# Optimization experiments

Measured on AMD Instinct MI355X. Metric: run time of the kernel, lower is better.

The kernel has to match this reference:

```python
import jax, jax.numpy as jnp
import numpy as np

N_NODES = 100000
N_EDGES = 3200000
IN_CH = 32
HID = 16


def setup_inputs() -> dict:
    key = jax.random.key(0)
    ks = jax.random.split(key, 8)
    x = jax.random.normal(ks[0], (N_NODES, IN_CH), dtype=jnp.float32)
    edge_index = jax.random.randint(ks[1], (2, N_EDGES), 0, N_NODES, dtype=jnp.int64)
    s1 = 1.0 / np.sqrt(IN_CH)
    s2 = 1.0 / np.sqrt(HID)
    Wl1 = jax.random.normal(ks[2], (HID, IN_CH), dtype=jnp.float32) * s1
    Wr1 = jax.random.normal(ks[3], (HID, IN_CH), dtype=jnp.float32) * s1
    b1 = jnp.zeros((HID,), dtype=jnp.float32)
    Wl2 = jax.random.normal(ks[4], (1, HID), dtype=jnp.float32) * s2
    Wr2 = jax.random.normal(ks[5], (1, HID), dtype=jnp.float32) * s2
    b2 = jnp.zeros((1,), dtype=jnp.float32)
    return {"x": x, "edge_index": edge_index, "Wl1": Wl1, "Wr1": Wr1,
            "b1": b1, "Wl2": Wl2, "Wr2": Wr2, "b2": b2}


def _sage_conv(h, src, dst, deg_inv, Wl, Wr, b):
    # mean aggregation of source features at destination nodes
    msg_sum = jax.ops.segment_sum(h[src], dst, num_segments=N_NODES)  # [N, F]
    agg = msg_sum * deg_inv[:, None]
    # lin_l(agg) + lin_r(h): lin_l carries the bias (PyG SAGEConv convention)
    return agg @ Wl.T + b + h @ Wr.T


def reference(x, edge_index, Wl1, Wr1, b1, Wl2, Wr2, b2):
    src = edge_index[0]
    dst = edge_index[1]
    deg = jax.ops.segment_sum(jnp.ones((N_EDGES,), dtype=x.dtype), dst,
                              num_segments=N_NODES)
    deg_inv = 1.0 / jnp.maximum(deg, 1.0)  # mean; nodes w/o in-edges get 0 agg

    h = _sage_conv(x, src, dst, deg_inv, Wl1, Wr1, b1)
    h = jax.nn.relu(h)
    # F.dropout in eval mode -> identity
    out = _sage_conv(h, src, dst, deg_inv, Wl2, Wr2, b2)
    return out.squeeze(-1)  # [N]
```

## Files before the change

### kernel.cpp

```cpp
#include <hip/hip_runtime.h>

#define N_NODES 100000
#define N_EDGES 3200000
#define NB 1024
#define BKN 98
#define RSZ 3968
#define TILE 6250
#define NTILES 512
#define MAXIT 13
#define MAXB 8


__device__ __forceinline__ float bf2f_lo(unsigned int w) {
  return __uint_as_float(w << 16);
}
__device__ __forceinline__ float bf2f_hi(unsigned int w) {
  return __uint_as_float(w & 0xFFFF0000u);
}
__device__ __forceinline__ unsigned short f2bf(float f) {
  unsigned int b = __float_as_uint(f);
  return (unsigned short)((b + 0x7FFFu + ((b >> 16) & 1u)) >> 16);
}

__global__ __launch_bounds__(256) void k_proj1(
    const float* __restrict__ x, const float* __restrict__ Wl1,
    const float* __restrict__ Wr1, const float* __restrict__ b1,
    unsigned short* __restrict__ p1h, float* __restrict__ q1b,
    int* __restrict__ gcur) {
  __shared__ float sWl[512];
  __shared__ float sWr[512];
  __shared__ float sb[16];
  const int t = threadIdx.x;
  if (t < 64) {
    const int gi = blockIdx.x * 64 + t;
    if (gi < NB * 16) gcur[gi] = 0;
  }
  for (int i = t; i < 512; i += 256) {
    sWl[i] = Wl1[i];
    sWr[i] = Wr1[i];
  }
  if (t < 16) sb[t] = b1[t];
  __syncthreads();

  const int n = blockIdx.x * 256 + t;
  if (n >= N_NODES) return;

  float xr[32];
  const float4* xp = (const float4*)(x + (size_t)n * 32);
#pragma unroll
  for (int j = 0; j < 8; ++j) {
    float4 v = xp[j];
    xr[4 * j + 0] = v.x;
    xr[4 * j + 1] = v.y;
    xr[4 * j + 2] = v.z;
    xr[4 * j + 3] = v.w;
  }
  float pv[16], qv[16];
#pragma unroll
  for (int hh = 0; hh < 16; ++hh) {
    float a = 0.f, b = 0.f;
#pragma unroll
    for (int i = 0; i < 32; ++i) {
      a = fmaf(xr[i], sWl[hh * 32 + i], a);
      b = fmaf(xr[i], sWr[hh * 32 + i], b);
    }
    pv[hh] = a;
    qv[hh] = b + sb[hh];
  }
  unsigned int w[8];
#pragma unroll
  for (int j = 0; j < 8; ++j)
    w[j] = (unsigned int)f2bf(pv[2 * j]) |
           ((unsigned int)f2bf(pv[2 * j + 1]) << 16);
  uint4* pp = (uint4*)(p1h + (size_t)n * 16);
  pp[0] = make_uint4(w[0], w[1], w[2], w[3]);
  pp[1] = make_uint4(w[4], w[5], w[6], w[7]);
  float4* qp = (float4*)(q1b + (size_t)n * 16);
#pragma unroll
  for (int j = 0; j < 4; ++j)
    qp[j] = make_float4(qv[4 * j], qv[4 * j + 1], qv[4 * j + 2], qv[4 * j + 3]);
}

__global__ __launch_bounds__(512) void k_bscatter(const int* __restrict__ ei,
                                                  int* __restrict__ gcur,
                                                  int* __restrict__ recs) {
  __shared__ int hist[1024];
  __shared__ int delta[NB];
  __shared__ int seg[512];
  __shared__ int stage[TILE];
  __shared__ unsigned short bid[TILE + 6];
  const int t = threadIdx.x;
  for (int i = t; i < 1024; i += 512) hist[i] = 0;
  __syncthreads();

  const int tb = blockIdx.x * TILE;
  int rec[MAXIT], aux[MAXIT];
#pragma unroll
  for (int i = 0; i < MAXIT; ++i) {
    const int pos = t + i * 512;
    if (pos < TILE) {
      const int e = tb + pos;
      const int s = ei[e];
      const int d = ei[N_EDGES + e];
      const int k = (int)((unsigned)d / (unsigned)BKN);
      const int rank = atomicAdd(&hist[k], 1);
      rec[i] = ((d - k * BKN) << 17) | s;
      aux[i] = (k << 16) | rank;
    } else {
      aux[i] = -1;
    }
  }
  __syncthreads();

  const int s0 = hist[2 * t], s1 = hist[2 * t + 1];
  const int my = s0 + s1;
  seg[t] = my;
  __syncthreads();
#pragma unroll
  for (int o = 1; o < 512; o <<= 1) {
    const int a = (t >= o) ? seg[t - o] : 0;
    __syncthreads();
    seg[t] += a;
    __syncthreads();
  }
  const int ex = seg[t] - my;
  hist[2 * t] = ex;
  hist[2 * t + 1] = ex + s0;
  {
    const int b = 2 * t;
    if (s0) delta[b] = b * RSZ + atomicAdd(&gcur[b * 16], s0) - ex;
    if (s1)
      delta[b + 1] =
          (b + 1) * RSZ + atomicAdd(&gcur[(b + 1) * 16], s1) - (ex + s0);
  }
  __syncthreads();

#pragma unroll
  for (int i = 0; i < MAXIT; ++i) {
    if (aux[i] >= 0) stage[hist[aux[i] >> 16] + (aux[i] & 0xFFFF)] = rec[i];
  }
  for (int k2 = t; k2 < NB; k2 += 512) {
    const int st = hist[k2];
    const int en = (k2 == NB - 1) ? TILE : hist[k2 + 1];
    for (int p = st; p < en; ++p) bid[p] = (unsigned short)k2;
  }
  __syncthreads();

  for (int pos = t; pos < TILE; pos += 512) {
    const int bb = bid[pos];
    const int idx = delta[bb] + pos;
    if (idx < (bb + 1) * RSZ) recs[idx] = stage[pos];
  }
}

__global__ __launch_bounds__(512, 8) void k_sortagg1(
    const int* __restrict__ gcur, const int* __restrict__ recs,
    const unsigned short* __restrict__ p1h, const float* __restrict__ q1b,
    const float* __restrict__ Wl2, const float* __restrict__ Wr2,
    float* __restrict__ p2, float* __restrict__ r2,
    float* __restrict__ deg_inv) {
  __shared__ int hist[128];
  __shared__ int nstart[128];
  __shared__ int ssort[RSZ];
  __shared__ float sWl[16], sWr[16];
  const int t = threadIdx.x;
  const int kb = blockIdx.x;
  const int b0 = kb * RSZ;
  const int gend = b0 + min(gcur[kb * 16], RSZ);
  if (t < 128) hist[t] = 0;
  if (t < 16) {
    sWl[t] = Wl2[t];
    sWr[t] = Wr2[t];
  }
  __syncthreads();

  int rc[MAXB], ax[MAXB];
#pragma unroll
  for (int i = 0; i < MAXB; ++i) {
    const int r = b0 + t + i * 512;
    if (r < gend) {
      const int rv = recs[r];
      const int local = rv >> 17;
      const int rank = atomicAdd(&hist[local], 1);
      rc[i] = rv & 0x1FFFF;
      ax[i] = (local << 13) | rank;
    } else {
      ax[i] = -1;
    }
  }
  __syncthreads();

  {
    const int v = (t < 128) ? hist[t] : 0;
    if (t < 128) nstart[t] = v;
    __syncthreads();
#pragma unroll
    for (int o = 1; o < 128; o <<= 1) {
      const int a = (t < 128 && t >= o) ? nstart[t - o] : 0;
      __syncthreads();
      if (t < 128) nstart[t] += a;
      __syncthreads();
    }
    if (t < 128) nstart[t] -= v;
  }
  __syncthreads();

#pragma unroll
  for (int i = 0; i < MAXB; ++i) {
    if (ax[i] >= 0) ssort[nstart[ax[i] >> 13] + (ax[i] & 0x1FFF)] = rc[i];
  }
  __syncthreads();

  const int quad = t & 3;
  const int half = quad & 1;
  const int epar = quad >> 1;
  const unsigned short* pb = p1h + half * 8;
  const int local = t >> 2;
  if (local < BKN) {
    const int n = kb * BKN + local;
    if (n < N_NODES) {
      const int st = nstart[local];
      const int k = hist[local];

      float acc[8];
#pragma unroll
      for (int i = 0; i < 8; ++i) acc[i] = 0.f;
      int j = epar;
      for (; j + 6 < k; j += 8) {
        const int s0 = ssort[st + j], s1 = ssort[st + j + 2],
                  s2 = ssort[st + j + 4], s3 = ssort[st + j + 6];
        const uint4 w0 = *(const uint4*)(pb + (size_t)s0 * 16);
        const uint4 w1 = *(const uint4*)(pb + (size_t)s1 * 16);
        const uint4 w2 = *(const uint4*)(pb + (size_t)s2 * 16);
        const uint4 w3 = *(const uint4*)(pb + (size_t)s3 * 16);
        acc[0] +=
            (bf2f_lo(w0.x) + bf2f_lo(w1.x)) + (bf2f_lo(w2.x) + bf2f_lo(w3.x));
        acc[1] +=
            (bf2f_hi(w0.x) + bf2f_hi(w1.x)) + (bf2f_hi(w2.x) + bf2f_hi(w3.x));
        acc[2] +=
            (bf2f_lo(w0.y) + bf2f_lo(w1.y)) + (bf2f_lo(w2.y) + bf2f_lo(w3.y));
        acc[3] +=
            (bf2f_hi(w0.y) + bf2f_hi(w1.y)) + (bf2f_hi(w2.y) + bf2f_hi(w3.y));
        acc[4] +=
            (bf2f_lo(w0.z) + bf2f_lo(w1.z)) + (bf2f_lo(w2.z) + bf2f_lo(w3.z));
        acc[5] +=
            (bf2f_hi(w0.z) + bf2f_hi(w1.z)) + (bf2f_hi(w2.z) + bf2f_hi(w3.z));
        acc[6] +=
            (bf2f_lo(w0.w) + bf2f_lo(w1.w)) + (bf2f_lo(w2.w) + bf2f_lo(w3.w));
        acc[7] +=
            (bf2f_hi(w0.w) + bf2f_hi(w1.w)) + (bf2f_hi(w2.w) + bf2f_hi(w3.w));
      }
      for (; j < k; j += 2) {
        const uint4 w = *(const uint4*)(pb + (size_t)ssort[st + j] * 16);
        acc[0] += bf2f_lo(w.x);
        acc[1] += bf2f_hi(w.x);
        acc[2] += bf2f_lo(w.y);
        acc[3] += bf2f_hi(w.y);
        acc[4] += bf2f_lo(w.z);
        acc[5] += bf2f_hi(w.z);
        acc[6] += bf2f_lo(w.w);
        acc[7] += bf2f_hi(w.w);
      }
#pragma unroll
      for (int i = 0; i < 8; ++i) acc[i] += __shfl_xor(acc[i], 2);

      const float di = 1.f / fmaxf((float)k, 1.f);
      const float4* qp = (const float4*)(q1b + (size_t)n * 16 + half * 8);
      const float4 qa = qp[0], qb = qp[1];
      float h[8];
      h[0] = fmaxf(fmaf(acc[0], di, qa.x), 0.f);
      h[1] = fmaxf(fmaf(acc[1], di, qa.y), 0.f);
      h[2] = fmaxf(fmaf(acc[2], di, qa.z), 0.f);
      h[3] = fmaxf(fmaf(acc[3], di, qa.w), 0.f);
      h[4] = fmaxf(fmaf(acc[4], di, qb.x), 0.f);
      h[5] = fmaxf(fmaf(acc[5], di, qb.y), 0.f);
      h[6] = fmaxf(fmaf(acc[6], di, qb.z), 0.f);
      h[7] = fmaxf(fmaf(acc[7], di, qb.w), 0.f);
      float pa = 0.f, pbv = 0.f;
#pragma unroll
      for (int i = 0; i < 8; ++i) {
        pa = fmaf(h[i], sWl[half * 8 + i], pa);
        pbv = fmaf(h[i], sWr[half * 8 + i], pbv);
      }
      pa += __shfl_xor(pa, 1);
      pbv += __shfl_xor(pbv, 1);
      if (quad == 0) {
        p2[n] = pa;
        r2[n] = pbv;
        deg_inv[n] = di;
      }
    }
  }
}

__global__ __launch_bounds__(512, 8) void k_agg2out(
    const int* __restrict__ gcur, const int* __restrict__ recs,
    const float* __restrict__ p2, const float* __restrict__ r2,
    const float* __restrict__ deg_inv, const float* __restrict__ b2,
    float* __restrict__ out) {
  __shared__ float acc[BKN];
  const int t = threadIdx.x;
  const int kb = blockIdx.x;
  if (t < BKN) acc[t] = 0.f;
  __syncthreads();

  const int b0 = kb * RSZ;
  const int cnt = min(gcur[kb * 16], RSZ);
  int r = t;
  for (; r + 1536 < cnt; r += 2048) {
    const int rv0 = recs[b0 + r];
    const int rv1 = recs[b0 + r + 512];
    const int rv2 = recs[b0 + r + 1024];
    const int rv3 = recs[b0 + r + 1536];
    const float v0 = p2[rv0 & 0x1FFFF];
    const float v1 = p2[rv1 & 0x1FFFF];
    const float v2 = p2[rv2 & 0x1FFFF];
    const float v3 = p2[rv3 & 0x1FFFF];
    atomicAdd(&acc[rv0 >> 17], v0);
    atomicAdd(&acc[rv1 >> 17], v1);
    atomicAdd(&acc[rv2 >> 17], v2);
    atomicAdd(&acc[rv3 >> 17], v3);
  }
  for (; r < cnt; r += 512) {
    const int rv = recs[b0 + r];
    atomicAdd(&acc[rv >> 17], p2[rv & 0x1FFFF]);
  }
  __syncthreads();

  if (t < BKN) {
    const int n = kb * BKN + t;
    if (n < N_NODES) out[n] = fmaf(acc[t], deg_inv[n], r2[n] + b2[0]);
  }
}

extern "C" void kernel_launch(void* const* d_in, const int* in_sizes, int n_in,
                              void* d_out, int out_size, void* d_ws,
                              size_t ws_size, hipStream_t stream) {
  const float* x   = (const float*)d_in[0];
  const int*   ei  = (const int*)d_in[1];
  const float* Wl1 = (const float*)d_in[2];
  const float* Wr1 = (const float*)d_in[3];
  const float* b1  = (const float*)d_in[4];
  const float* Wl2 = (const float*)d_in[5];
  const float* Wr2 = (const float*)d_in[6];
  const float* b2  = (const float*)d_in[7];
  float* out = (float*)d_out;

  const size_t N = N_NODES;
  int* wi = (int*)d_ws;
  int* gcur = wi;
  int* recs = wi + NB * 16;
  unsigned short* p1h = (unsigned short*)(recs + (size_t)NB * RSZ);
  float* q1b     = (float*)(p1h + 16 * N);
  float* p2      = q1b + 16 * N;
  float* r2      = p2 + N;
  float* deg_inv = r2 + N;

  k_proj1<<<(N_NODES + 255) / 256, 256, 0, stream>>>(x, Wl1, Wr1, b1, p1h,
                                                     q1b, gcur);
  k_bscatter<<<NTILES, 512, 0, stream>>>(ei, gcur, recs);
  k_sortagg1<<<NB, 512, 0, stream>>>(gcur, recs, p1h, q1b, Wl2, Wr2, p2, r2,
                                     deg_inv);
  k_agg2out<<<NB, 512, 0, stream>>>(gcur, recs, p2, r2, deg_inv, b2, out);
}
```

Baseline: 172.0 us.

## Fuse projection into edge bucket scatter and streamline scans and gather loops

Merges the layer-1 projection kernel into the edge-bucketing scatter kernel, sharing LDS through a union and overlapping x loads with edge reads. The gcur reset moves to a hipMemsetAsync. Block-wide LDS prefix scans are replaced with wavefront shuffle scans, and sortagg1 now uses 8 threads per node (two node passes) instead of 4. agg2out reads records as vectorized nontemporal int4 loads. The aim is fewer launches, fewer barriers and more memory parallelism, at the cost of higher register pressure in the fused kernel and an extra memset call.

```diff
diff --git a/kernel.cpp b/kernel.cpp
--- a/kernel.cpp
+++ b/kernel.cpp
@@ -9,6 +9,10 @@
 #define NTILES 512
 #define MAXIT 13
 #define MAXB 8
+#define PRN 196
+
+typedef int   i32x4 __attribute__((ext_vector_type(4)));
+typedef float f32x4 __attribute__((ext_vector_type(4)));
 
 
 __device__ __forceinline__ float bf2f_lo(unsigned int w) {
@@ -22,78 +26,37 @@
   return (unsigned short)((b + 0x7FFFu + ((b >> 16) & 1u)) >> 16);
 }
 
-__global__ __launch_bounds__(256) void k_proj1(
-    const float* __restrict__ x, const float* __restrict__ Wl1,
-    const float* __restrict__ Wr1, const float* __restrict__ b1,
-    unsigned short* __restrict__ p1h, float* __restrict__ q1b,
-    int* __restrict__ gcur) {
-  __shared__ float sWl[512];
-  __shared__ float sWr[512];
-  __shared__ float sb[16];
-  const int t = threadIdx.x;
-  if (t < 64) {
-    const int gi = blockIdx.x * 64 + t;
-    if (gi < NB * 16) gcur[gi] = 0;
-  }
-  for (int i = t; i < 512; i += 256) {
-    sWl[i] = Wl1[i];
-    sWr[i] = Wr1[i];
-  }
-  if (t < 16) sb[t] = b1[t];
-  __syncthreads();
-
-  const int n = blockIdx.x * 256 + t;
-  if (n >= N_NODES) return;
-
-  float xr[32];
-  const float4* xp = (const float4*)(x + (size_t)n * 32);
-#pragma unroll
-  for (int j = 0; j < 8; ++j) {
-    float4 v = xp[j];
-    xr[4 * j + 0] = v.x;
-    xr[4 * j + 1] = v.y;
-    xr[4 * j + 2] = v.z;
-    xr[4 * j + 3] = v.w;
-  }
-  float pv[16], qv[16];
-#pragma unroll
-  for (int hh = 0; hh < 16; ++hh) {
-    float a = 0.f, b = 0.f;
-#pragma unroll
-    for (int i = 0; i < 32; ++i) {
-      a = fmaf(xr[i], sWl[hh * 32 + i], a);
-      b = fmaf(xr[i], sWr[hh * 32 + i], b);
-    }
-    pv[hh] = a;
-    qv[hh] = b + sb[hh];
-  }
-  unsigned int w[8];
-#pragma unroll
-  for (int j = 0; j < 8; ++j)
-    w[j] = (unsigned int)f2bf(pv[2 * j]) |
-           ((unsigned int)f2bf(pv[2 * j + 1]) << 16);
-  uint4* pp = (uint4*)(p1h + (size_t)n * 16);
-  pp[0] = make_uint4(w[0], w[1], w[2], w[3]);
-  pp[1] = make_uint4(w[4], w[5], w[6], w[7]);
-  float4* qp = (float4*)(q1b + (size_t)n * 16);
-#pragma unroll
-  for (int j = 0; j < 4; ++j)
-    qp[j] = make_float4(qv[4 * j], qv[4 * j + 1], qv[4 * j + 2], qv[4 * j + 3]);
-}
-
-__global__ __launch_bounds__(512) void k_bscatter(const int* __restrict__ ei,
-                                                  int* __restrict__ gcur,
-                                                  int* __restrict__ recs) {
+__global__ __launch_bounds__(512, 4) void k_projscatter(
+    const float* __restrict__ x, const int* __restrict__ ei,
+    const float* __restrict__ Wl1, const float* __restrict__ Wr1,
+    const float* __restrict__ b1, unsigned short* __restrict__ p1h,
+    float* __restrict__ q1b, int* __restrict__ gcur, int* __restrict__ recs) {
   __shared__ int hist[1024];
   __shared__ int delta[NB];
-  __shared__ int seg[512];
-  __shared__ int stage[TILE];
-  __shared__ unsigned short bid[TILE + 6];
+  __shared__ int wsum[8];
+  __shared__ union {
+    struct { float Wl[512], Wr[512], b[16]; } w;
+    struct { int stage[TILE]; unsigned short bid[TILE + 6]; } s;
+  } u;
   const int t = threadIdx.x;
+  const int kb = blockIdx.x;
+
   for (int i = t; i < 1024; i += 512) hist[i] = 0;
-  __syncthreads();
-
-  const int tb = blockIdx.x * TILE;
+  u.w.Wl[t] = Wl1[t];
+  u.w.Wr[t] = Wr1[t];
+  if (t < 16) u.w.b[t] = b1[t];
+  __syncthreads();
+
+  const int n = kb * PRN + t;
+  f32x4 xv[8];
+  const bool do_proj = (t < PRN) && (n < N_NODES);
+  if (do_proj) {
+    const f32x4* xp = (const f32x4*)(x + (size_t)n * 32);
+#pragma unroll
+    for (int j = 0; j < 8; ++j) xv[j] = xp[j];
+  }
+
+  const int tb = kb * TILE;
   int rec[MAXIT], aux[MAXIT];
 #pragma unroll
   for (int i = 0; i < MAXIT; ++i) {
@@ -110,20 +73,58 @@
       aux[i] = -1;
     }
   }
+
+  if (do_proj) {
+    float pv[16], qv[16];
+#pragma unroll
+    for (int hh = 0; hh < 16; ++hh) {
+      float a = 0.f, b = 0.f;
+#pragma unroll
+      for (int i = 0; i < 32; ++i) {
+        const float xi = xv[i >> 2][i & 3];
+        a = fmaf(xi, u.w.Wl[hh * 32 + i], a);
+        b = fmaf(xi, u.w.Wr[hh * 32 + i], b);
+      }
+      pv[hh] = a;
+      qv[hh] = b + u.w.b[hh];
+    }
+    unsigned int w[8];
+#pragma unroll
+    for (int j = 0; j < 8; ++j)
+      w[j] = (unsigned int)f2bf(pv[2 * j]) |
+             ((unsigned int)f2bf(pv[2 * j + 1]) << 16);
+    uint4* pp = (uint4*)(p1h + (size_t)n * 16);
+    pp[0] = make_uint4(w[0], w[1], w[2], w[3]);
+    pp[1] = make_uint4(w[4], w[5], w[6], w[7]);
+    float4* qp = (float4*)(q1b + (size_t)n * 16);
+#pragma unroll
+    for (int j = 0; j < 4; ++j)
+      qp[j] =
+          make_float4(qv[4 * j], qv[4 * j + 1], qv[4 * j + 2], qv[4 * j + 3]);
+  }
   __syncthreads();
 
   const int s0 = hist[2 * t], s1 = hist[2 * t + 1];
-  const int my = s0 + s1;
-  seg[t] = my;
-  __syncthreads();
-#pragma unroll
-  for (int o = 1; o < 512; o <<= 1) {
-    const int a = (t >= o) ? seg[t - o] : 0;
-    __syncthreads();
-    seg[t] += a;
-    __syncthreads();
-  }
-  const int ex = seg[t] - my;
+  const int sp = s0 + s1;
+  int incl = sp;
+#pragma unroll
+  for (int o = 1; o < 64; o <<= 1) {
+    const int uu = __shfl_up(incl, o);
+    if ((t & 63) >= o) incl += uu;
+  }
+  if ((t & 63) == 63) wsum[t >> 6] = incl;
+  __syncthreads();
+  if (t == 0) {
+    int run = 0;
+#pragma unroll
+    for (int i = 0; i < 8; ++i) {
+      const int v = wsum[i];
+      wsum[i] = run;
+      run += v;
+    }
+  }
+  __syncthreads();
+  const int ex = wsum[t >> 6] + incl - sp;
   hist[2 * t] = ex;
   hist[2 * t + 1] = ex + s0;
   {
@@ -137,19 +138,20 @@
 
 #pragma unroll
   for (int i = 0; i < MAXIT; ++i) {
-    if (aux[i] >= 0) stage[hist[aux[i] >> 16] + (aux[i] & 0xFFFF)] = rec[i];
+    if (aux[i] >= 0)
+      u.s.stage[hist[aux[i] >> 16] + (aux[i] & 0xFFFF)] = rec[i];
   }
   for (int k2 = t; k2 < NB; k2 += 512) {
     const int st = hist[k2];
     const int en = (k2 == NB - 1) ? TILE : hist[k2 + 1];
-    for (int p = st; p < en; ++p) bid[p] = (unsigned short)k2;
+    for (int p = st; p < en; ++p) u.s.bid[p] = (unsigned short)k2;
   }
   __syncthreads();
 
   for (int pos = t; pos < TILE; pos += 512) {
-    const int bb = bid[pos];
+    const int bb = u.s.bid[pos];
     const int idx = delta[bb] + pos;
-    if (idx < (bb + 1) * RSZ) recs[idx] = stage[pos];
+    if (idx < (bb + 1) * RSZ) recs[idx] = u.s.stage[pos];
   }
 }
 
@@ -166,7 +168,7 @@
   const int t = threadIdx.x;
   const int kb = blockIdx.x;
   const int b0 = kb * RSZ;
-  const int gend = b0 + min(gcur[kb * 16], RSZ);
+  const int cnt = min(gcur[kb * 16], RSZ);
   if (t < 128) hist[t] = 0;
   if (t < 16) {
     sWl[t] = Wl2[t];
@@ -177,9 +179,9 @@
   int rc[MAXB], ax[MAXB];
 #pragma unroll
   for (int i = 0; i < MAXB; ++i) {
-    const int r = b0 + t + i * 512;
-    if (r < gend) {
-      const int rv = recs[r];
+    const int r = t + i * 512;
+    if (r < cnt) {
+      const int rv = __builtin_nontemporal_load(recs + b0 + r);
       const int local = rv >> 17;
       const int rank = atomicAdd(&hist[local], 1);
       rc[i] = rv & 0x1FFFF;
@@ -190,18 +192,21 @@
   }
   __syncthreads();
 
-  {
-    const int v = (t < 128) ? hist[t] : 0;
-    if (t < 128) nstart[t] = v;
-    __syncthreads();
-#pragma unroll
-    for (int o = 1; o < 128; o <<= 1) {
-      const int a = (t < 128 && t >= o) ? nstart[t - o] : 0;
-      __syncthreads();
-      if (t < 128) nstart[t] += a;
-      __syncthreads();
-    }
-    if (t < 128) nstart[t] -= v;
+  if (t < 64) {
+    const int a = hist[t], b = hist[t + 64];
+    int ia = a, ib = b;
+#pragma unroll
+    for (int o = 1; o < 64; o <<= 1) {
+      const int ua = __shfl_up(ia, o);
+      const int ub = __shfl_up(ib, o);
+      if (t >= o) {
+        ia += ua;
+        ib += ub;
+      }
+    }
+    const int tot = __shfl(ia, 63);
+    nstart[t] = ia - a;
+    nstart[t + 64] = tot + ib - b;
   }
   __syncthreads();
 
@@ -211,71 +216,78 @@
   }
   __syncthreads();
 
-  const int quad = t & 3;
-  const int half = quad & 1;
-  const int epar = quad >> 1;
+  const int oct = t & 7;
+  const int half = oct & 1;
+  const int epar = oct >> 1;
   const unsigned short* pb = p1h + half * 8;
-  const int local = t >> 2;
-  if (local < BKN) {
+#pragma unroll
+  for (int p = 0; p < 2; ++p) {
+    const int local = p * 64 + (t >> 3);
+    if (local >= BKN) continue;
     const int n = kb * BKN + local;
-    if (n < N_NODES) {
-      const int st = nstart[local];
-      const int k = hist[local];
-
-      float acc[8];
-#pragma unroll
-      for (int i = 0; i < 8; ++i) acc[i] = 0.f;
-      int j = epar;
-      for (; j + 6 < k; j += 8) {
-        const int s0 = ssort[st + j], s1 = ssort[st + j + 2],
-                  s2 = ssort[st + j + 4], s3 = ssort[st + j + 6];
-        const uint4 w0 = *(const uint4*)(pb + (size_t)s0 * 16);
-        const uint4 w1 = *(const uint4*)(pb + (size_t)s1 * 16);
-        const uint4 w2 = *(const uint4*)(pb + (size_t)s2 * 16);
-        const uint4 w3 = *(const uint4*)(pb + (size_t)s3 * 16);
-        acc[0] +=
-            (bf2f_lo(w0.x) + bf2f_lo(w1.x)) + (bf2f_lo(w2.x) + bf2f_lo(w3.x));
-        acc[1] +=
-            (bf2f_hi(w0.x) + bf2f_hi(w1.x)) + (bf2f_hi(w2.x) + bf2f_hi(w3.x));
-        acc[2] +=
-            (bf2f_lo(w0.y) + bf2f_lo(w1.y)) + (bf2f_lo(w2.y) + bf2f_lo(w3.y));
-        acc[3] +=
-            (bf2f_hi(w0.y) + bf2f_hi(w1.y)) + (bf2f_hi(w2.y) + bf2f_hi(w3.y));
-        acc[4] +=
-            (bf2f_lo(w0.z) + bf2f_lo(w1.z)) + (bf2f_lo(w2.z) + bf2f_lo(w3.z));
-        acc[5] +=
-            (bf2f_hi(w0.z) + bf2f_hi(w1.z)) + (bf2f_hi(w2.z) + bf2f_hi(w3.z));
-        acc[6] +=
-            (bf2f_lo(w0.w) + bf2f_lo(w1.w)) + (bf2f_lo(w2.w) + bf2f_lo(w3.w));
-        acc[7] +=
-            (bf2f_hi(w0.w) + bf2f_hi(w1.w)) + (bf2f_hi(w2.w) + bf2f_hi(w3.w));
-      }
-      for (; j < k; j += 2) {
-        const uint4 w = *(const uint4*)(pb + (size_t)ssort[st + j] * 16);
-        acc[0] += bf2f_lo(w.x);
-        acc[1] += bf2f_hi(w.x);
-        acc[2] += bf2f_lo(w.y);
-        acc[3] += bf2f_hi(w.y);
-        acc[4] += bf2f_lo(w.z);
-        acc[5] += bf2f_hi(w.z);
-        acc[6] += bf2f_lo(w.w);
-        acc[7] += bf2f_hi(w.w);
-      }
-#pragma unroll
-      for (int i = 0; i < 8; ++i) acc[i] += __shfl_xor(acc[i], 2);
-
+    if (n >= N_NODES) continue;
+    const int st = nstart[local];
+    const int k = hist[local];
+
+    float acc[8];
+#pragma unroll
+    for (int i = 0; i < 8; ++i) acc[i] = 0.f;
+    int j = epar;
+    for (; j + 12 < k; j += 16) {
+      const int s0 = ssort[st + j], s1 = ssort[st + j + 4],
+                s2 = ssort[st + j + 8], s3 = ssort[st + j + 12];
+      const uint4 w0 = *(const uint4*)(pb + (size_t)s0 * 16);
+      const uint4 w1 = *(const uint4*)(pb + (size_t)s1 * 16);
+      const uint4 w2 = *(const uint4*)(pb + (size_t)s2 * 16);
+      const uint4 w3 = *(const uint4*)(pb + (size_t)s3 * 16);
+      acc[0] +=
+          (bf2f_lo(w0.x) + bf2f_lo(w1.x)) + (bf2f_lo(w2.x) + bf2f_lo(w3.x));
+      acc[1] +=
+          (bf2f_hi(w0.x) + bf2f_hi(w1.x)) + (bf2f_hi(w2.x) + bf2f_hi(w3.x));
+      acc[2] +=
+          (bf2f_lo(w0.y) + bf2f_lo(w1.y)) + (bf2f_lo(w2.y) + bf2f_lo(w3.y));
+      acc[3] +=
+          (bf2f_hi(w0.y) + bf2f_hi(w1.y)) + (bf2f_hi(w2.y) + bf2f_hi(w3.y));
+      acc[4] +=
+          (bf2f_lo(w0.z) + bf2f_lo(w1.z)) + (bf2f_lo(w2.z) + bf2f_lo(w3.z));
+      acc[5] +=
+          (bf2f_hi(w0.z) + bf2f_hi(w1.z)) + (bf2f_hi(w2.z) + bf2f_hi(w3.z));
+      acc[6] +=
+          (bf2f_lo(w0.w) + bf2f_lo(w1.w)) + (bf2f_lo(w2.w) + bf2f_lo(w3.w));
+      acc[7] +=
+          (bf2f_hi(w0.w) + bf2f_hi(w1.w)) + (bf2f_hi(w2.w) + bf2f_hi(w3.w));
+    }
+    for (; j < k; j += 4) {
+      const uint4 w = *(const uint4*)(pb + (size_t)ssort[st + j] * 16);
+      acc[0] += bf2f_lo(w.x);
+      acc[1] += bf2f_hi(w.x);
+      acc[2] += bf2f_lo(w.y);
+      acc[3] += bf2f_hi(w.y);
+      acc[4] += bf2f_lo(w.z);
+      acc[5] += bf2f_hi(w.z);
+      acc[6] += bf2f_lo(w.w);
+      acc[7] += bf2f_hi(w.w);
+    }
+#pragma unroll
+    for (int i = 0; i < 8; ++i) {
+      acc[i] += __shfl_xor(acc[i], 2);
+      acc[i] += __shfl_xor(acc[i], 4);
+    }
+
+    if (epar == 0) {
       const float di = 1.f / fmaxf((float)k, 1.f);
-      const float4* qp = (const float4*)(q1b + (size_t)n * 16 + half * 8);
-      const float4 qa = qp[0], qb = qp[1];
+      const f32x4* qp = (const f32x4*)(q1b + (size_t)n * 16 + half * 8);
+      const f32x4 qa = __builtin_nontemporal_load(qp);
+      const f32x4 qb = __builtin_nontemporal_load(qp + 1);
       float h[8];
-      h[0] = fmaxf(fmaf(acc[0], di, qa.x), 0.f);
-      h[1] = fmaxf(fmaf(acc[1], di, qa.y), 0.f);
-      h[2] = fmaxf(fmaf(acc[2], di, qa.z), 0.f);
-      h[3] = fmaxf(fmaf(acc[3], di, qa.w), 0.f);
-      h[4] = fmaxf(fmaf(acc[4], di, qb.x), 0.f);
-      h[5] = fmaxf(fmaf(acc[5], di, qb.y), 0.f);
-      h[6] = fmaxf(fmaf(acc[6], di, qb.z), 0.f);
-      h[7] = fmaxf(fmaf(acc[7], di, qb.w), 0.f);
+      h[0] = fmaxf(fmaf(acc[0], di, qa[0]), 0.f);
+      h[1] = fmaxf(fmaf(acc[1], di, qa[1]), 0.f);
+      h[2] = fmaxf(fmaf(acc[2], di, qa[2]), 0.f);
+      h[3] = fmaxf(fmaf(acc[3], di, qa[3]), 0.f);
+      h[4] = fmaxf(fmaf(acc[4], di, qb[0]), 0.f);
+      h[5] = fmaxf(fmaf(acc[5], di, qb[1]), 0.f);
+      h[6] = fmaxf(fmaf(acc[6], di, qb[2]), 0.f);
+      h[7] = fmaxf(fmaf(acc[7], di, qb[3]), 0.f);
       float pa = 0.f, pbv = 0.f;
 #pragma unroll
       for (int i = 0; i < 8; ++i) {
@@ -284,7 +296,7 @@
       }
       pa += __shfl_xor(pa, 1);
       pbv += __shfl_xor(pbv, 1);
-      if (quad == 0) {
+      if (half == 0) {
         p2[n] = pa;
         r2[n] = pbv;
         deg_inv[n] = di;
@@ -306,30 +318,31 @@
 
   const int b0 = kb * RSZ;
   const int cnt = min(gcur[kb * 16], RSZ);
-  int r = t;
-  for (; r + 1536 < cnt; r += 2048) {
-    const int rv0 = recs[b0 + r];
-    const int rv1 = recs[b0 + r + 512];
-    const int rv2 = recs[b0 + r + 1024];
-    const int rv3 = recs[b0 + r + 1536];
-    const float v0 = p2[rv0 & 0x1FFFF];
-    const float v1 = p2[rv1 & 0x1FFFF];
-    const float v2 = p2[rv2 & 0x1FFFF];
-    const float v3 = p2[rv3 & 0x1FFFF];
-    atomicAdd(&acc[rv0 >> 17], v0);
-    atomicAdd(&acc[rv1 >> 17], v1);
-    atomicAdd(&acc[rv2 >> 17], v2);
-    atomicAdd(&acc[rv3 >> 17], v3);
-  }
-  for (; r < cnt; r += 512) {
-    const int rv = recs[b0 + r];
-    atomicAdd(&acc[rv >> 17], p2[rv & 0x1FFFF]);
+  for (int base = 4 * t; base < cnt; base += 2048) {
+    const i32x4 rv =
+        __builtin_nontemporal_load((const i32x4*)(recs + b0 + base));
+    if (base + 3 < cnt) {
+      const float v0 = p2[rv[0] & 0x1FFFF];
+      const float v1 = p2[rv[1] & 0x1FFFF];
+      const float v2 = p2[rv[2] & 0x1FFFF];
+      const float v3 = p2[rv[3] & 0x1FFFF];
+      atomicAdd(&acc[rv[0] >> 17], v0);
+      atomicAdd(&acc[rv[1] >> 17], v1);
+      atomicAdd(&acc[rv[2] >> 17], v2);
+      atomicAdd(&acc[rv[3] >> 17], v3);
+    } else {
+#pragma unroll
+      for (int e2 = 0; e2 < 4; ++e2) {
+        if (base + e2 < cnt)
+          atomicAdd(&acc[rv[e2] >> 17], p2[rv[e2] & 0x1FFFF]);
+      }
+    }
   }
   __syncthreads();
 
   if (t < BKN) {
-    const int n = kb * BKN + t;
-    if (n < N_NODES) out[n] = fmaf(acc[t], deg_inv[n], r2[n] + b2[0]);
+    const int nn = kb * BKN + t;
+    if (nn < N_NODES) out[nn] = fmaf(acc[t], deg_inv[nn], r2[nn] + b2[0]);
   }
 }
 
@@ -356,9 +369,9 @@
   float* r2      = p2 + N;
   float* deg_inv = r2 + N;
 
-  k_proj1<<<(N_NODES + 255) / 256, 256, 0, stream>>>(x, Wl1, Wr1, b1, p1h,
-                                                     q1b, gcur);
-  k_bscatter<<<NTILES, 512, 0, stream>>>(ei, gcur, recs);
+  hipMemsetAsync(gcur, 0, NB * 16 * sizeof(int), stream);
+  k_projscatter<<<NTILES, 512, 0, stream>>>(x, ei, Wl1, Wr1, b1, p1h, q1b,
+                                            gcur, recs);
   k_sortagg1<<<NB, 512, 0, stream>>>(gcur, recs, p1h, q1b, Wl2, Wr2, p2, r2,
                                      deg_inv);
   k_agg2out<<<NB, 512, 0, stream>>>(gcur, recs, p2, r2, deg_inv, b2, out);
```

After: 179.5 us. +4.3%, slower.
